# Kernel tuning notes

Measured on AMD Instinct MI355X. Metric: run time of the kernel, lower is better.

## Reference

```python
import jax, jax.numpy as jnp
import numpy as np


def _conv1x1(x, w, b):
    # x: (B, C, H, W), w: (O, C), b: (O,) -> (B, O, H, W)
    return jnp.einsum('bchw,oc->bohw', x, w) + b[None, :, None, None]


def setup_inputs() -> dict:
    key = jax.random.key(0)
    ks = jax.random.split(key, 9)
    C, Cb = 256, 128
    B, H, W = 4, 64, 64
    s_in = 1.0 / np.sqrt(C)   # kaiming-uniform-ish scale for 1x1 convs
    s_bn = 1.0 / np.sqrt(Cb)
    return {
        'x': jax.random.normal(ks[0], (B, C, H, W), dtype=jnp.float32),
        'theta_w': jax.random.uniform(ks[1], (Cb, C), jnp.float32, -s_in, s_in),
        'theta_b': jax.random.uniform(ks[2], (Cb,), jnp.float32, -s_in, s_in),
        'phi_w': jax.random.uniform(ks[3], (Cb, C), jnp.float32, -s_in, s_in),
        'phi_b': jax.random.uniform(ks[4], (Cb,), jnp.float32, -s_in, s_in),
        'g_w': jax.random.uniform(ks[5], (Cb, C), jnp.float32, -s_in, s_in),
        'g_b': jax.random.uniform(ks[6], (Cb,), jnp.float32, -s_in, s_in),
        'W_w': jax.random.uniform(ks[7], (C, Cb), jnp.float32, -s_bn, s_bn),
        'W_b': jax.random.uniform(ks[8], (C,), jnp.float32, -s_bn, s_bn),
    }


def reference(x, theta_w, theta_b, phi_w, phi_b, g_w, g_b, W_w, W_b):
    B, C, H, Wd = x.shape
    Cb = theta_w.shape[0]
    # NOTE: the original uses raw torch.reshape (row-major), NOT transpose,
    # so (B, Cb, H, W) -> (B, H*W, Cb) scrambles channel/spatial layout.
    # We replicate that exactly with jnp.reshape.
    theta = _conv1x1(x, theta_w, theta_b).reshape(B, -1, Cb)   # (B, N, Cb)
    phi = _conv1x1(x, phi_w, phi_b).reshape(B, Cb, -1)         # (B, Cb, N)
    g = _conv1x1(x, g_w, g_b).reshape(B, -1, Cb)               # (B, N, Cb)
    scores = jnp.einsum('bnc,bcm->bnm', theta, phi)            # (B, N, N)
    attn = jax.nn.softmax(scores, axis=1)                      # softmax over dim=1 (unusual axis)
    y = jnp.einsum('bnm,bmc->bnc', attn, g)                    # (B, N, Cb)
    y = y.reshape(B, -1, H, Wd)                                # raw reshape back to (B, Cb, H, W)
    w = _conv1x1(y, W_w, W_b)                                  # (B, C, H, W)
    return w + x
```

## Files before the change

### kernel.cpp

```cpp
#include <hip/hip_runtime.h>
#include <math.h>

constexpr int CI = 256;
constexpr int CB = 128;
constexpr int HWD = 4096;
constexpr int NBATCH = 4;
constexpr int NN_ = 4096;
constexpr size_t U1 = (size_t)NBATCH * NN_ * CB;
constexpr size_t U_THETA = 0;
constexpr size_t U_PHIT  = U1;
constexpr size_t U_G     = 2 * U1;
constexpr size_t U_GT    = 3 * U1;
constexpr size_t U_Y     = 4 * U1;
constexpr size_t U_XT    = 4 * U1;
constexpr size_t U_WCAT  = 8 * U1;
constexpr size_t U_WW    = 8 * U1 + 98304;
constexpr size_t F_D     = (8 * U1 + 131072) / 2;

typedef short v8s __attribute__((ext_vector_type(8)));
typedef unsigned short u8s __attribute__((ext_vector_type(8)));
typedef unsigned int v4u __attribute__((ext_vector_type(4)));
typedef float v4f __attribute__((ext_vector_type(4)));
typedef float v16f __attribute__((ext_vector_type(16)));
#define MFMA16(a, b, c) __builtin_amdgcn_mfma_f32_16x16x32_bf16(a, b, c, 0, 0, 0)
#define MFMA32(a, b, c) __builtin_amdgcn_mfma_f32_32x32x16_bf16(a, b, c, 0, 0, 0)

__device__ __forceinline__ unsigned short f2bf(float f) {
    union { float f; unsigned u; } v; v.f = f;
    unsigned r = v.u + 0x7fff + ((v.u >> 16) & 1);
    return (unsigned short)(r >> 16);
}
__device__ __forceinline__ float bf2f(unsigned short s) {
    union { unsigned u; float f; } v; v.u = (unsigned)s << 16;
    return v.f;
}
__device__ __forceinline__ unsigned pack2bf(float lo, float hi) {
    return (unsigned)f2bf(lo) | ((unsigned)f2bf(hi) << 16);
}
__device__ __forceinline__ void pl32swap(unsigned &a, unsigned &b) {
    asm volatile("v_permlane32_swap_b32 %0, %1" : "+v"(a), "+v"(b));
}
__device__ __forceinline__ v8s pack_swap(float p0, float p1, float p2, float p3,
                                         float p4, float p5, float p6, float p7) {
    unsigned c0 = pack2bf(p0, p1), c1 = pack2bf(p2, p3);
    unsigned c2 = pack2bf(p4, p5), c3 = pack2bf(p6, p7);
    pl32swap(c0, c2);
    pl32swap(c1, c3);
    union { v4u u; v8s s; } r;
    r.u[0] = c0; r.u[1] = c1; r.u[2] = c2; r.u[3] = c3;
    return r.s;
}

__global__ __launch_bounds__(256) void k0_xpose(
    const float* __restrict__ x, unsigned short* __restrict__ xT,
    const float* __restrict__ tw, const float* __restrict__ pw,
    const float* __restrict__ gw, const float* __restrict__ Ww,
    unsigned short* __restrict__ wcat, unsigned short* __restrict__ wwB)
{
    __shared__ unsigned short T[64 * 72];
    const int t = threadIdx.x;
    if (blockIdx.y == 4) {
        int wb = blockIdx.x + 64 * blockIdx.z;
        if (t < 128) {
            int e = (wb * 128 + t) * 4;
            const float* src; unsigned short* dst;
            if (e < 32768)       { src = tw + e;           dst = wcat + e; }
            else if (e < 65536)  { src = pw + (e - 32768); dst = wcat + e; }
            else if (e < 98304)  { src = gw + (e - 65536); dst = wcat + e; }
            else                 { src = Ww + (e - 98304); dst = wwB + (e - 98304); }
            float4 f = *(const float4*)src;
            ushort4 u;
            u.x = f2bf(f.x); u.y = f2bf(f.y); u.z = f2bf(f.z); u.w = f2bf(f.w);
            *(ushort4*)dst = u;
        }
        return;
    }
    const int hw0 = blockIdx.x * 64, c0 = blockIdx.y * 64, b = blockIdx.z;
    const float* xb = x + (size_t)b * CI * HWD;
    const int rr = t >> 4, cc = t & 15;
    #pragma unroll
    for (int pass = 0; pass < 4; pass++) {
        float4 f = *(const float4*)&xb[(size_t)(c0 + pass * 16 + rr) * HWD + hw0 + cc * 4];
        T[(cc * 4 + 0) * 72 + pass * 16 + rr] = f2bf(f.x);
        T[(cc * 4 + 1) * 72 + pass * 16 + rr] = f2bf(f.y);
        T[(cc * 4 + 2) * 72 + pass * 16 + rr] = f2bf(f.z);
        T[(cc * 4 + 3) * 72 + pass * 16 + rr] = f2bf(f.w);
    }
    __syncthreads();
    const int row = t >> 2, cs = (t & 3) * 16;
    unsigned short* dst = xT + (size_t)b * NN_ * CI;
    #pragma unroll
    for (int h = 0; h < 2; h++)
        *(u8s*)&dst[(size_t)(hw0 + row) * CI + c0 + cs + h * 8] =
            *(const u8s*)&T[row * 72 + cs + h * 8];
}

__global__ __launch_bounds__(256, 4) void k1_mfma(
    const unsigned short* __restrict__ xT, const unsigned short* __restrict__ wcat,
    const float* __restrict__ tb, const float* __restrict__ pb,
    const float* __restrict__ gb,
    unsigned short* __restrict__ thetaB, unsigned short* __restrict__ phiTB,
    unsigned short* __restrict__ gB)
{
    __shared__ unsigned short LdsX[64 * 268];
    unsigned short* T = LdsX;
    const int t = threadIdx.x;
    const int lane = t & 63, w = t >> 6;
    const int l31 = lane & 31, lh = lane >> 5;
    const int qj = w >> 1, qh = w & 1;
    const int hw0 = blockIdx.x * 64, j0 = blockIdx.y * 64, b = blockIdx.z;
    const int matId = j0 >> 7, jl0 = j0 & 127;
    const float* bvec = (matId == 0) ? tb : (matId == 1) ? pb : gb;
    const unsigned short* xb = xT + (size_t)b * NN_ * CI;

    {
        const int row = t >> 2, seg = t & 3;
        #pragma unroll
        for (int c8 = 0; c8 < 8; c8++)
            *(u8s*)&LdsX[row * 268 + seg * 64 + c8 * 8] =
                *(const u8s*)&xb[(size_t)(hw0 + row) * CI + seg * 64 + c8 * 8];
    }
    __syncthreads();

    v16f s = {};
    #pragma unroll
    for (int kt = 0; kt < 16; kt++) {
        v8s a = *(const v8s*)&wcat[(size_t)(j0 + qj * 32 + l31) * CI + kt * 16 + lh * 8];
        v8s bx = *(const v8s*)&LdsX[(qh * 32 + l31) * 268 + kt * 16 + lh * 8];
        s = MFMA32(a, bx, s);
    }

    if (matId != 1) {
        unsigned short* dst = ((matId == 0) ? thetaB : gB) + (size_t)b * CB * HWD;
        #pragma unroll
        for (int reg = 0; reg < 16; reg++) {
            int row = (reg & 3) + 8 * (reg >> 2) + 4 * lh;
            int cb = jl0 + qj * 32 + row;
            dst[(size_t)cb * HWD + hw0 + qh * 32 + l31] = f2bf(s[reg] + bvec[cb]);
        }
    } else {
        __syncthreads();
        #pragma unroll
        for (int reg = 0; reg < 16; reg++) {
            int row = (reg & 3) + 8 * (reg >> 2) + 4 * lh;
            T[(qh * 32 + l31) * 76 + qj * 32 + row] =
                f2bf(s[reg] + bvec[jl0 + qj * 32 + row]);
        }
        __syncthreads();
        unsigned short* dst = phiTB + (size_t)b * NN_ * CB;
        const int row = t >> 2, cs = (t & 3) * 16;
        #pragma unroll
        for (int h = 0; h < 2; h++)
            *(u8s*)&dst[(size_t)(hw0 + row) * CB + jl0 + cs + h * 8] =
                *(const u8s*)&T[row * 76 + cs + h * 8];
    }
}

__global__ __launch_bounds__(256, 2) void k2_colsum(
    const unsigned short* __restrict__ thetaB,
    const unsigned short* __restrict__ phiTB,
    float* __restrict__ Dout)
{
    __shared__ float part[4][128];
    const int t = threadIdx.x;
    const int lane = t & 63, w = t >> 6;
    const int ln = lane & 15, quad = lane >> 4;
    const int m0 = blockIdx.x * 128, q = blockIdx.y, b = blockIdx.z;
    const unsigned short* th = thetaB + (size_t)b * NN_ * CB;
    const unsigned short* ph = phiTB + (size_t)b * NN_ * CB;

    v8s bf[8][4];
    #pragma unroll
    for (int mt = 0; mt < 8; mt++)
        #pragma unroll
        for (int kt = 0; kt < 4; kt++)
            bf[mt][kt] = *(const v8s*)&ph[(size_t)(m0 + mt * 16 + ln) * CB + kt * 32 + quad * 8];

    float dsum[8] = {};
    const int nBeg = q * 1024 + w * 16, nEnd = q * 1024 + 1024;
    v8s af[4], afn[4];
    #pragma unroll
    for (int kt = 0; kt < 4; kt++)
        af[kt] = *(const v8s*)&th[(size_t)(nBeg + ln) * CB + kt * 32 + quad * 8];
    for (int n0 = nBeg; n0 < nEnd; n0 += 64) {
        int nn = (n0 + 64 < nEnd) ? n0 + 64 : nBeg;
        #pragma unroll
        for (int kt = 0; kt < 4; kt++)
            afn[kt] = *(const v8s*)&th[(size_t)(nn + ln) * CB + kt * 32 + quad * 8];
        #pragma unroll
        for (int mt = 0; mt < 8; mt++) {
            v4f s = {};
            #pragma unroll
            for (int kt = 0; kt < 4; kt++)
                s = MFMA16(af[kt], bf[mt][kt], s);
            #pragma unroll
            for (int r = 0; r < 4; r++)
                dsum[mt] += __expf(s[r]);
        }
        #pragma unroll
        for (int kt = 0; kt < 4; kt++) af[kt] = afn[kt];
    }
    #pragma unroll
    for (int mt = 0; mt < 8; mt++) {
        float v = dsum[mt];
        v += __shfl_xor(v, 16);
        v += __shfl_xor(v, 32);
        dsum[mt] = v;
    }
    if (quad == 0) {
        #pragma unroll
        for (int mt = 0; mt < 8; mt++) part[w][mt * 16 + ln] = dsum[mt];
    }
    __syncthreads();
    if (t < 128) {
        float v = part[0][t] + part[1][t] + part[2][t] + part[3][t];
        Dout[((size_t)q * NBATCH + b) * NN_ + m0 + t] = v;
    }
}

__global__ __launch_bounds__(256) void k1b_transpose_scale_g(
    const unsigned short* __restrict__ gB, const float* __restrict__ D,
    unsigned short* __restrict__ gTB)
{
    __shared__ unsigned short T[128 * 36];
    const int t = threadIdx.x;
    const int m0 = blockIdx.x * 32;
    const int b  = blockIdx.z;
    const unsigned short* F = gB + (size_t)b * CB * HWD;
    unsigned short* dst = gTB + (size_t)b * CB * HWD;
    const int mrow = t >> 3, cg = t & 7;
    {
        int m = m0 + mrow;
        float d = D[((size_t)0 * NBATCH + b) * NN_ + m]
                + D[((size_t)1 * NBATCH + b) * NN_ + m]
                + D[((size_t)2 * NBATCH + b) * NN_ + m]
                + D[((size_t)3 * NBATCH + b) * NN_ + m];
        float r = 1.0f / d;
        #pragma unroll
        for (int j8 = 0; j8 < 2; j8++) {
            int cbase = cg * 8 + j8 * 64;
            u8s u = *(const u8s*)&F[(size_t)m * CB + cbase];
            #pragma unroll
            for (int e = 0; e < 8; e++)
                T[(cbase + e) * 36 + mrow] = f2bf(bf2f(u[e]) * r);
        }
    }
    __syncthreads();
    const int c = t >> 1, mh = (t & 1) * 16;
    #pragma unroll
    for (int h8 = 0; h8 < 2; h8++)
        *(u8s*)&dst[(size_t)c * HWD + m0 + mh + h8 * 8] =
            *(const u8s*)&T[c * 36 + mh + h8 * 8];
}

__global__ __launch_bounds__(512, 2) void k3_attn(
    const unsigned short* __restrict__ thetaB,
    const unsigned short* __restrict__ phiTB,
    const unsigned short* __restrict__ gTB,
    unsigned short* __restrict__ Y)
{
    __shared__ unsigned short Lphi[2][2][64 * 134];
    const int t = threadIdx.x;
    const int lane = t & 63;
    const int w = (t >> 6) & 3;
    const int g = t >> 8;
    const int l31 = lane & 31, lh = lane >> 5;
    const int tl = t & 255;
    const int rowS = tl >> 4, colS = tl & 15;
    const int n0 = blockIdx.x * 128, q = blockIdx.y, b = blockIdx.z;
    const unsigned short* th = thetaB + (size_t)b * NN_ * CB;
    const unsigned short* ph = phiTB + (size_t)b * NN_ * CB;
    const unsigned short* gT = gTB + (size_t)b * CB * HWD;

    v8s ath[8];
    #pragma unroll
    for (int kt = 0; kt < 8; kt++)
        ath[kt] = *(const v8s*)&th[(size_t)(n0 + w * 32 + l31) * CB + kt * 16 + lh * 8];

    const int mBeg = q * 1024 + g * 512;
    v8s preg[4];
    #pragma unroll
    for (int p = 0; p < 4; p++)
        preg[p] = *(const v8s*)&ph[(size_t)(mBeg + p * 16 + rowS) * CB + colS * 8];
    #pragma unroll
    for (int p = 0; p < 4; p++)
        *(v8s*)&Lphi[g][0][(p * 16 + rowS) * 134 + colS * 8] = preg[p];
    #pragma unroll
    for (int p = 0; p < 4; p++)
        preg[p] = *(const v8s*)&ph[(size_t)(mBeg + 64 + p * 16 + rowS) * CB + colS * 8];
    __syncthreads();

    v16f yacc[4] = {};
    #pragma unroll 2
    for (int it = 0; it < 8; ++it) {
        const int cur = it & 1;
        const int m0 = mBeg + it * 64;
        v8s gfA[2][4];
        #pragma unroll
        for (int ks = 0; ks < 2; ks++)
            #pragma unroll
            for (int ct = 0; ct < 4; ct++)
                gfA[ks][ct] = *(const v8s*)&gT[(size_t)(ct * 32 + l31) * HWD + m0 + ks * 16 + lh * 8];
        v16f st0 = {}, st1 = {};
        #pragma unroll
        for (int kt = 0; kt < 8; kt++) {
            v8s a0 = *(const v8s*)&Lphi[g][cur][(l31) * 134 + kt * 16 + lh * 8];
            v8s a1 = *(const v8s*)&Lphi[g][cur][(32 + l31) * 134 + kt * 16 + lh * 8];
            st0 = MFMA32(a0, ath[kt], st0);
            st1 = MFMA32(a1, ath[kt], st1);
        }
        #pragma unroll
        for (int p = 0; p < 4; p++)
            *(v8s*)&Lphi[g][cur ^ 1][(p * 16 + rowS) * 134 + colS * 8] = preg[p];
        __syncthreads();
        {
            const int mP = mBeg + ((it + 2) & 7) * 64;
            #pragma unroll
            for (int p = 0; p < 4; p++)
                preg[p] = *(const v8s*)&ph[(size_t)(mP + p * 16 + rowS) * CB + colS * 8];
        }
        v8s gfB[2][4];
        #pragma unroll
        for (int ks = 0; ks < 2; ks++)
            #pragma unroll
            for (int ct = 0; ct < 4; ct++)
                gfB[ks][ct] = *(const v8s*)&gT[(size_t)(ct * 32 + l31) * HWD + m0 + 32 + ks * 16 + lh * 8];
        v8s apv0 = pack_swap(__expf(st0[0]),  __expf(st0[1]),  __expf(st0[2]),  __expf(st0[3]),
                             __expf(st0[4]),  __expf(st0[5]),  __expf(st0[6]),  __expf(st0[7]));
        v8s apv1 = pack_swap(__expf(st0[8]),  __expf(st0[9]),  __expf(st0[10]), __expf(st0[11]),
                             __expf(st0[12]), __expf(st0[13]), __expf(st0[14]), __expf(st0[15]));
        v8s apv2 = pack_swap(__expf(st1[0]),  __expf(st1[1]),  __expf(st1[2]),  __expf(st1[3]),
                             __expf(st1[4]),  __expf(st1[5]),  __expf(st1[6]),  __expf(st1[7]));
        v8s apv3 = pack_swap(__expf(st1[8]),  __expf(st1[9]),  __expf(st1[10]), __expf(st1[11]),
                             __expf(st1[12]), __expf(st1[13]), __expf(st1[14]), __expf(st1[15]));
        #pragma unroll
        for (int ct = 0; ct < 4; ct++) yacc[ct] = MFMA32(apv0, gfA[0][ct], yacc[ct]);
        #pragma unroll
        for (int ct = 0; ct < 4; ct++) yacc[ct] = MFMA32(apv1, gfA[1][ct], yacc[ct]);
        #pragma unroll
        for (int ct = 0; ct < 4; ct++) yacc[ct] = MFMA32(apv2, gfB[0][ct], yacc[ct]);
        #pragma unroll
        for (int ct = 0; ct < 4; ct++) yacc[ct] = MFMA32(apv3, gfB[1][ct], yacc[ct]);
    }
    float* red = (float*)&Lphi[0][0][0];
    if (g == 1) {
        #pragma unroll
        for (int ct = 0; ct < 4; ct++)
            #pragma unroll
            for (int reg = 0; reg < 16; reg++)
                red[w * 4096 + (ct * 16 + reg) * 64 + lane] = yacc[ct][reg];
    }
    __syncthreads();
    if (g == 0) {
        unsigned short* yp = Y + ((size_t)q * NBATCH + b) * CB * HWD;
        #pragma unroll
        for (int ct = 0; ct < 4; ct++)
            #pragma unroll
            for (int reg = 0; reg < 16; reg++) {
                float v = yacc[ct][reg] + red[w * 4096 + (ct * 16 + reg) * 64 + lane];
                int row = (reg & 3) + 8 * (reg >> 2) + 4 * lh;
                yp[(size_t)(n0 + w * 32 + row) * CB + ct * 32 + l31] = f2bf(v);
            }
    }
}

__global__ __launch_bounds__(256, 2) void k4_mfma(
    const float* __restrict__ x, const unsigned short* __restrict__ wwB,
    const float* __restrict__ Wb, const unsigned short* __restrict__ Ybuf,
    float* __restrict__ out)
{
    __shared__ unsigned short Yt[64 * 136];
    const int t = threadIdx.x;
    const int lane = t & 63, w = t >> 6;
    const int ln = lane & 15, quad = lane >> 4;
    const int hw0 = blockIdx.x * 64, o0 = blockIdx.y * 128, b = blockIdx.z;

    const int cb = t >> 1, seg = (t & 1) * 32;
    #pragma unroll
    for (int g8 = 0; g8 < 4; g8++) {
        float sum[8] = {};
        #pragma unroll
        for (int q = 0; q < 4; q++) {
            u8s u = *(const u8s*)&Ybuf[((size_t)q * NBATCH + b) * CB * HWD +
                                       (size_t)cb * HWD + hw0 + seg + g8 * 8];
            #pragma unroll
            for (int j = 0; j < 8; j++) sum[j] += bf2f(u[j]);
        }
        #pragma unroll
        for (int j = 0; j < 8; j++)
            Yt[(seg + g8 * 8 + j) * 136 + cb] = f2bf(sum[j]);
    }
    __syncthreads();

    v8s aw[2][4];
    #pragma unroll
    for (int os = 0; os < 2; os++)
        #pragma unroll
        for (int kt = 0; kt < 4; kt++)
            aw[os][kt] = *(const v8s*)&wwB[(size_t)(o0 + w * 32 + os * 16 + ln) * CB + kt * 32 + quad * 8];

    v4f s[2][4] = {};
    #pragma unroll
    for (int kt = 0; kt < 4; kt++) {
        v8s by[4];
        #pragma unroll
        for (int mt = 0; mt < 4; mt++)
            by[mt] = *(const v8s*)&Yt[(mt * 16 + ln) * 136 + kt * 32 + quad * 8];
        #pragma unroll
        for (int os = 0; os < 2; os++)
            #pragma unroll
            for (int mt = 0; mt < 4; mt++)
                s[os][mt] = MFMA16(aw[os][kt], by[mt], s[os][mt]);
    }
    #pragma unroll
    for (int os = 0; os < 2; os++)
        #pragma unroll
        for (int mt = 0; mt < 4; mt++)
            #pragma unroll
            for (int r = 0; r < 4; r++) {
                int o = o0 + w * 32 + os * 16 + quad * 4 + r;
                size_t idx = (size_t)b * CI * HWD + (size_t)o * HWD + hw0 + mt * 16 + ln;
                out[idx] = s[os][mt][r] + Wb[o] + x[idx];
            }
}

extern "C" void kernel_launch(void* const* d_in, const int* in_sizes, int n_in,
                              void* d_out, int out_size, void* d_ws, size_t ws_size,
                              hipStream_t stream)
{
    const float* x  = (const float*)d_in[0];
    const float* tw = (const float*)d_in[1];
    const float* tb = (const float*)d_in[2];
    const float* pw = (const float*)d_in[3];
    const float* pb = (const float*)d_in[4];
    const float* gw = (const float*)d_in[5];
    const float* gb = (const float*)d_in[6];
    const float* Ww = (const float*)d_in[7];
    const float* Wb = (const float*)d_in[8];
    unsigned short* wsu = (unsigned short*)d_ws;
    float* wsf = (float*)d_ws;
    unsigned short* thetaB = wsu + U_THETA;
    unsigned short* phiTB  = wsu + U_PHIT;
    unsigned short* gB     = wsu + U_G;
    unsigned short* gTB    = wsu + U_GT;
    unsigned short* Ybuf   = wsu + U_Y;
    unsigned short* xTB    = wsu + U_XT;
    unsigned short* wcatB  = wsu + U_WCAT;
    unsigned short* wwB    = wsu + U_WW;
    float* Dbuf = wsf + F_D;
    float* out = (float*)d_out;
    dim3 blk(256, 1, 1);
    dim3 blk512(512, 1, 1);
    hipLaunchKernelGGL(k0_xpose, dim3(64, 5, NBATCH), blk, 0, stream,
                       x, xTB, tw, pw, gw, Ww, wcatB, wwB);
    hipLaunchKernelGGL(k1_mfma, dim3(64, 6, NBATCH), blk, 0, stream,
                       xTB, wcatB, tb, pb, gb, thetaB, phiTB, gB);
    hipLaunchKernelGGL(k2_colsum, dim3(32, 4, NBATCH), blk, 0, stream,
                       thetaB, phiTB, Dbuf);
    hipLaunchKernelGGL(k1b_transpose_scale_g, dim3(128, 1, NBATCH), blk, 0, stream,
                       gB, Dbuf, gTB);
    hipLaunchKernelGGL(k3_attn, dim3(32, 4, NBATCH), blk512, 0, stream,
                       thetaB, phiTB, gTB, Ybuf);
    hipLaunchKernelGGL(k4_mfma, dim3(64, 2, NBATCH), blk, 0, stream,
                       x, wwB, Wb, Ybuf, out);
}
```

Measured before the change: 216.2 us.

## Stage gT tiles through LDS with coalesced loads, single-buffer phi

Measured after the change: 297.0 us. 37.4% more time.

```diff
diff --git a/kernel.cpp b/kernel.cpp
--- a/kernel.cpp
+++ b/kernel.cpp
@@ -259,7 +259,7 @@
     const unsigned short* __restrict__ gTB,
     unsigned short* __restrict__ Y)
 {
-    __shared__ unsigned short Lphi[2][2][64 * 134];
+    __shared__ unsigned short Lds[2][17024];
     const int t = threadIdx.x;
     const int lane = t & 63;
     const int w = (t >> 6) & 3;
@@ -267,10 +267,13 @@
     const int l31 = lane & 31, lh = lane >> 5;
     const int tl = t & 255;
     const int rowS = tl >> 4, colS = tl & 15;
+    const int gRow = tl >> 3, gCol = (tl & 7) * 8;
     const int n0 = blockIdx.x * 128, q = blockIdx.y, b = blockIdx.z;
     const unsigned short* th = thetaB + (size_t)b * NN_ * CB;
     const unsigned short* ph = phiTB + (size_t)b * NN_ * CB;
     const unsigned short* gT = gTB + (size_t)b * CB * HWD;
+    unsigned short* Lphi = &Lds[g][0];
+    unsigned short* Lg   = &Lds[g][8576];
 
     v8s ath[8];
     #pragma unroll
@@ -284,47 +287,27 @@
         preg[p] = *(const v8s*)&ph[(size_t)(mBeg + p * 16 + rowS) * CB + colS * 8];
     #pragma unroll
     for (int p = 0; p < 4; p++)
-        *(v8s*)&Lphi[g][0][(p * 16 + rowS) * 134 + colS * 8] = preg[p];
+        *(v8s*)&Lphi[(p * 16 + rowS) * 134 + colS * 8] = preg[p];
     #pragma unroll
     for (int p = 0; p < 4; p++)
         preg[p] = *(const v8s*)&ph[(size_t)(mBeg + 64 + p * 16 + rowS) * CB + colS * 8];
     __syncthreads();
 
     v16f yacc[4] = {};
-    #pragma unroll 2
     for (int it = 0; it < 8; ++it) {
-        const int cur = it & 1;
         const int m0 = mBeg + it * 64;
-        v8s gfA[2][4];
-        #pragma unroll
-        for (int ks = 0; ks < 2; ks++)
-            #pragma unroll
-            for (int ct = 0; ct < 4; ct++)
-                gfA[ks][ct] = *(const v8s*)&gT[(size_t)(ct * 32 + l31) * HWD + m0 + ks * 16 + lh * 8];
+        v8s gst[4];
+        #pragma unroll
+        for (int j = 0; j < 4; j++)
+            gst[j] = *(const v8s*)&gT[(size_t)(j * 32 + gRow) * HWD + m0 + gCol];
         v16f st0 = {}, st1 = {};
         #pragma unroll
         for (int kt = 0; kt < 8; kt++) {
-            v8s a0 = *(const v8s*)&Lphi[g][cur][(l31) * 134 + kt * 16 + lh * 8];
-            v8s a1 = *(const v8s*)&Lphi[g][cur][(32 + l31) * 134 + kt * 16 + lh * 8];
+            v8s a0 = *(const v8s*)&Lphi[(l31) * 134 + kt * 16 + lh * 8];
+            v8s a1 = *(const v8s*)&Lphi[(32 + l31) * 134 + kt * 16 + lh * 8];
             st0 = MFMA32(a0, ath[kt], st0);
             st1 = MFMA32(a1, ath[kt], st1);
         }
-        #pragma unroll
-        for (int p = 0; p < 4; p++)
-            *(v8s*)&Lphi[g][cur ^ 1][(p * 16 + rowS) * 134 + colS * 8] = preg[p];
-        __syncthreads();
-        {
-            const int mP = mBeg + ((it + 2) & 7) * 64;
-            #pragma unroll
-            for (int p = 0; p < 4; p++)
-                preg[p] = *(const v8s*)&ph[(size_t)(mP + p * 16 + rowS) * CB + colS * 8];
-        }
-        v8s gfB[2][4];
-        #pragma unroll
-        for (int ks = 0; ks < 2; ks++)
-            #pragma unroll
-            for (int ct = 0; ct < 4; ct++)
-                gfB[ks][ct] = *(const v8s*)&gT[(size_t)(ct * 32 + l31) * HWD + m0 + 32 + ks * 16 + lh * 8];
         v8s apv0 = pack_swap(__expf(st0[0]),  __expf(st0[1]),  __expf(st0[2]),  __expf(st0[3]),
                              __expf(st0[4]),  __expf(st0[5]),  __expf(st0[6]),  __expf(st0[7]));
         v8s apv1 = pack_swap(__expf(st0[8]),  __expf(st0[9]),  __expf(st0[10]), __expf(st0[11]),
@@ -333,16 +316,43 @@
                              __expf(st1[4]),  __expf(st1[5]),  __expf(st1[6]),  __expf(st1[7]));
         v8s apv3 = pack_swap(__expf(st1[8]),  __expf(st1[9]),  __expf(st1[10]), __expf(st1[11]),
                              __expf(st1[12]), __expf(st1[13]), __expf(st1[14]), __expf(st1[15]));
-        #pragma unroll
-        for (int ct = 0; ct < 4; ct++) yacc[ct] = MFMA32(apv0, gfA[0][ct], yacc[ct]);
-        #pragma unroll
-        for (int ct = 0; ct < 4; ct++) yacc[ct] = MFMA32(apv1, gfA[1][ct], yacc[ct]);
-        #pragma unroll
-        for (int ct = 0; ct < 4; ct++) yacc[ct] = MFMA32(apv2, gfB[0][ct], yacc[ct]);
-        #pragma unroll
-        for (int ct = 0; ct < 4; ct++) yacc[ct] = MFMA32(apv3, gfB[1][ct], yacc[ct]);
-    }
-    float* red = (float*)&Lphi[0][0][0];
+        __syncthreads();
+        #pragma unroll
+        for (int p = 0; p < 4; p++)
+            *(v8s*)&Lphi[(p * 16 + rowS) * 134 + colS * 8] = preg[p];
+        #pragma unroll
+        for (int j = 0; j < 4; j++)
+            *(v8s*)&Lg[(j * 32 + gRow) * 66 + gCol] = gst[j];
+        __syncthreads();
+        {
+            const int mP = mBeg + ((it + 2) & 7) * 64;
+            #pragma unroll
+            for (int p = 0; p < 4; p++)
+                preg[p] = *(const v8s*)&ph[(size_t)(mP + p * 16 + rowS) * CB + colS * 8];
+        }
+        #pragma unroll
+        for (int ct = 0; ct < 4; ct++) {
+            v8s b0 = *(const v8s*)&Lg[(ct * 32 + l31) * 66 + 0 + lh * 8];
+            yacc[ct] = MFMA32(apv0, b0, yacc[ct]);
+        }
+        #pragma unroll
+        for (int ct = 0; ct < 4; ct++) {
+            v8s b1 = *(const v8s*)&Lg[(ct * 32 + l31) * 66 + 16 + lh * 8];
+            yacc[ct] = MFMA32(apv1, b1, yacc[ct]);
+        }
+        #pragma unroll
+        for (int ct = 0; ct < 4; ct++) {
+            v8s b2 = *(const v8s*)&Lg[(ct * 32 + l31) * 66 + 32 + lh * 8];
+            yacc[ct] = MFMA32(apv2, b2, yacc[ct]);
+        }
+        #pragma unroll
+        for (int ct = 0; ct < 4; ct++) {
+            v8s b3 = *(const v8s*)&Lg[(ct * 32 + l31) * 66 + 48 + lh * 8];
+            yacc[ct] = MFMA32(apv3, b3, yacc[ct]);
+        }
+    }
+    __syncthreads();
+    float* red = (float*)&Lds[0][0];
     if (g == 1) {
         #pragma unroll
         for (int ct = 0; ct < 4; ct++)
```
